# Optimization experiments

Hardware: AMD Instinct MI355X
Metric: run time of the kernel (lower is better)

## Reference

```python
import jax, jax.numpy as jnp
import numpy as np


def setup_inputs() -> dict:
    key = jax.random.key(0)
    k1, k2 = jax.random.split(key)
    B, S, D = 8, 4096, 1024
    E, P = 8, 4
    x = jax.random.normal(k1, (B, S, D), dtype=jnp.float32)
    phi_kernel = jax.random.normal(k2, (D, E * P), dtype=jnp.float32) * (1.0 / np.sqrt(D))
    phi_bias = jnp.zeros((E * P,), dtype=jnp.float32)
    return {"x": x, "phi_kernel": phi_kernel, "phi_bias": phi_bias,
            "num_experts": E, "num_slots": P}


def reference(x, phi_kernel, phi_bias, num_experts, num_slots):
    B, S, D = x.shape
    E, P = num_experts, num_slots
    # phi logits: [B,S,E,P]
    phi_logits = (jnp.einsum('bsd,dk->bsk', x, phi_kernel) + phi_bias).reshape(B, S, E, P)
    # softmax over the sequence axis (each slot is a convex combo of tokens)
    phi_weights = jax.nn.softmax(phi_logits, axis=1)
    # soft slots: weighted sum over tokens -> [B,E,P,D] (fused, no [B,S,E,P,D] blowup)
    soft_slots = jnp.einsum('bsd,bsep->bepd', x, phi_weights)
    expert_inputs = soft_slots.reshape(B, E, P * D)
    expert_weights = jnp.full((B, S, E), 1.0 / E, dtype=x.dtype)
    expert_indices = jnp.broadcast_to(jnp.arange(E, dtype=jnp.int32)[None, None, :], (B, S, E))
    return (expert_weights, expert_indices, phi_weights, soft_slots, expert_inputs)
```

## Files before the change

kernel.cpp:

```cpp
#include <hip/hip_runtime.h>
#include <hip/hip_bf16.h>

#define B 8
#define S 4096
#define DD 1024
#define KK 32

typedef __attribute__((ext_vector_type(8))) short bf16x8;
typedef __attribute__((ext_vector_type(16))) float f32x16;

static __device__ __forceinline__ unsigned short f2bf(float f) {
    unsigned int u = __builtin_bit_cast(unsigned int, f);
    u += 0x7FFFu + ((u >> 16) & 1u);
    return (unsigned short)(u >> 16);
}

static __device__ __forceinline__ unsigned int pack2bf(float lo, float hi) {
    return (unsigned int)f2bf(lo) | ((unsigned int)f2bf(hi) << 16);
}

static __device__ __forceinline__ void gload_lds16(const void* g, void* l) {
    __builtin_amdgcn_global_load_lds(
        (const __attribute__((address_space(1))) unsigned int*)g,
        (__attribute__((address_space(3))) unsigned int*)l, 16, 0, 0);
}

__global__ __launch_bounds__(256) void k0_phit(const float* __restrict__ phi,
                                               unsigned short* __restrict__ phiT) {
    __shared__ float lt[32][33];
    const int d0 = blockIdx.x * 32;
    const int tid = threadIdx.x;
#pragma unroll
    for (int i = 0; i < 4; ++i) {
        int slot = tid + i * 256;
        int d = slot >> 5, k = slot & 31;
        lt[d][k] = phi[(size_t)(d0 + d) * KK + k];
    }
    __syncthreads();
    const int k = tid >> 3, c = tid & 7, d = c * 4;
    short4 pk;
    pk.x = (short)f2bf(lt[d + 0][k]);
    pk.y = (short)f2bf(lt[d + 1][k]);
    pk.z = (short)f2bf(lt[d + 2][k]);
    pk.w = (short)f2bf(lt[d + 3][k]);
    *(short4*)(phiT + (size_t)k * DD + d0 + d) = pk;
}

__global__ __launch_bounds__(256) void k1_logits(const float* __restrict__ x,
                                                 const unsigned short* __restrict__ phiT,
                                                 const float* __restrict__ bias,
                                                 float* __restrict__ lp,
                                                 float* __restrict__ pmax,
                                                 float* __restrict__ psum) {
    __shared__ __align__(16) char sm[65536];

    const int bid = blockIdx.x;
    const int st = bid & 31;
    const int b  = bid >> 5;
    const int tid = threadIdx.x;
    const int wv = __builtin_amdgcn_readfirstlane(tid >> 6);
    const int lane = tid & 63;
    const int l31 = lane & 31;
    const int half = lane >> 5;

    {
        const uint4* pg = (const uint4*)phiT;
#pragma unroll
        for (int i = 0; i < 16; ++i) {
            int slot = tid + i * 256;
            int k = slot >> 7, blk = slot & 127;
            uint4 v = pg[(size_t)k * 128 + blk];
            *(uint4*)(sm + (size_t)k * 2048 + ((blk ^ (k & 7)) << 4)) = v;
        }
    }

    f32x16 acc;
    {
        float bv = bias[l31];
#pragma unroll
        for (int r = 0; r < 16; ++r) acc[r] = bv;
    }
    __syncthreads();

    const float* xg = x + ((size_t)(b * S + st * 128 + wv * 32 + l31)) * DD + half * 8;
    const int kx = l31 & 7;
    const char* brow = sm + (size_t)l31 * 2048;

#pragma unroll 8
    for (int ch = 0; ch < 64; ++ch) {
        float4 a0 = *(const float4*)(xg + ch * 16);
        float4 a1 = *(const float4*)(xg + ch * 16 + 4);
        unsigned int p0 = pack2bf(a0.x, a0.y);
        unsigned int p1 = pack2bf(a0.z, a0.w);
        unsigned int p2 = pack2bf(a1.x, a1.y);
        unsigned int p3 = pack2bf(a1.z, a1.w);
        uint4 pv = make_uint4(p0, p1, p2, p3);
        bf16x8 af = __builtin_bit_cast(bf16x8, pv);
        bf16x8 bfv = *(const bf16x8*)(brow + (((ch * 2 + half) ^ kx) << 4));
        acc = __builtin_amdgcn_mfma_f32_32x32x16_bf16(af, bfv, acc, 0, 0, 0);
    }

    __syncthreads();
    float* lt = (float*)sm;
#pragma unroll
    for (int r = 0; r < 16; ++r) {
        int row = (r & 3) + 8 * (r >> 2) + 4 * half;
        lt[(size_t)l31 * 129 + wv * 32 + row] = acc[r];
    }
    __syncthreads();

    float* o = lp + ((size_t)b * KK) * S + st * 128;
#pragma unroll
    for (int i = 0; i < 4; ++i) {
        int slot = tid + i * 256;
        int k = slot >> 5, s4 = slot & 31;
        float4 v;
        v.x = lt[k * 129 + s4 * 4 + 0];
        v.y = lt[k * 129 + s4 * 4 + 1];
        v.z = lt[k * 129 + s4 * 4 + 2];
        v.w = lt[k * 129 + s4 * 4 + 3];
        *(float4*)(o + (size_t)k * S + s4 * 4) = v;
    }

    const int pk = tid >> 3, pj = tid & 7;
    const float* lr = lt + (size_t)pk * 129 + pj * 16;
    float m = lr[0];
#pragma unroll
    for (int i = 1; i < 16; ++i) m = fmaxf(m, lr[i]);
#pragma unroll
    for (int off = 4; off >= 1; off >>= 1) m = fmaxf(m, __shfl_xor(m, off, 64));
    float l = 0.f;
#pragma unroll
    for (int i = 0; i < 16; ++i) l += __expf(lr[i] - m);
#pragma unroll
    for (int off = 4; off >= 1; off >>= 1) l += __shfl_xor(l, off, 64);
    if (pj == 0) {
        pmax[((size_t)b * KK + pk) * 32 + st] = m;
        psum[((size_t)b * KK + pk) * 32 + st] = l;
    }
}

__global__ __launch_bounds__(256) void k2c_norm(const float* __restrict__ lp,
                                                const float* __restrict__ pmax,
                                                const float* __restrict__ psum,
                                                unsigned short* __restrict__ wbT,
                                                float* __restrict__ pw_out) {
    __shared__ float tile[128][33];
    __shared__ float sM[32], sLinv[32];
    const int b  = blockIdx.x >> 5;
    const int sc = blockIdx.x & 31;
    const int s0 = sc * 128;
    const int tid = threadIdx.x;

    if (tid < 32) {
        const int k = tid;
        float M = -1e30f, L = 0.f;
#pragma unroll
        for (int c = 0; c < 32; ++c) {
            float mc = pmax[((size_t)b * KK + k) * 32 + c];
            float lc = psum[((size_t)b * KK + k) * 32 + c];
            float nM = fmaxf(M, mc);
            L = L * __expf(M - nM) + lc * __expf(mc - nM);
            M = nM;
        }
        sM[k] = M;
        sLinv[k] = 1.0f / L;
    }
    __syncthreads();

    const int sL = tid & 127;
    const int kh = tid >> 7;
#pragma unroll
    for (int kk = 0; kk < 16; ++kk) {
        const int k = kk * 2 + kh;
        const size_t idx = ((size_t)b * KK + k) * S + s0 + sL;
        float v = lp[idx];
        float w = __expf(v - sM[k]) * sLinv[k];
        wbT[idx] = f2bf(w);
        tile[sL][k] = w;
    }
    __syncthreads();

    float* ob = pw_out + ((size_t)b * S + s0) * KK;
#pragma unroll
    for (int i = 0; i < 4; ++i) {
        const int idx4 = tid + i * 256;
        const int sl = idx4 >> 3, kq = idx4 & 7;
        float4 v4 = make_float4(tile[sl][kq * 4 + 0], tile[sl][kq * 4 + 1],
                                tile[sl][kq * 4 + 2], tile[sl][kq * 4 + 3]);
        ((float4*)ob)[idx4] = v4;
    }
}

__global__ __launch_bounds__(256) void k3_slots(const float* __restrict__ x,
                                                const unsigned short* __restrict__ wbT,
                                                float* __restrict__ part) {
    __shared__ __align__(16) char sm[2 * 32768 + 2 * 4096];

    const int bid = blockIdx.x;
    const int sc = bid & 7;
    const int dg = (bid >> 3) & 7;
    const int b  = bid >> 6;
    const int tid = threadIdx.x;
    const int wv = __builtin_amdgcn_readfirstlane(tid >> 6);
    const int lane = tid & 63;
    const int l31 = lane & 31;
    const int half = lane >> 5;

    const char* xsrc = (const char*)(x + ((size_t)(b * S + sc * 512 + wv * 16 + half)) * DD
                                       + dg * 128 + l31 * 4);
    const int wk = wv * 8 + (lane >> 3);
    const char* wsrc = (const char*)wbT + ((size_t)(b * KK + wk) * S + sc * 512) * 2
                                        + (((lane & 7) ^ (wk & 7)) << 4);

    char* const xb0 = sm;
    char* const wb0 = sm + 65536;

    auto stage = [&](int ch, int buf) {
        char* xb = xb0 + buf * 32768 + wv * (16 * 512);
        const char* xs = xsrc + (size_t)ch * (64 * DD * 4);
#pragma unroll
        for (int t = 0; t < 8; ++t)
            gload_lds16(xs + (size_t)t * (2 * DD * 4), xb + t * 1024);
        gload_lds16(wsrc + (size_t)ch * 128, wb0 + buf * 4096 + wv * 1024);
    };

    f32x16 acc;
#pragma unroll
    for (int r = 0; r < 16; ++r) acc[r] = 0.f;

    stage(0, 0);
    __syncthreads();

    const int col = wv * 32 + l31;
    const int kx = l31 & 7;

    for (int ch = 0; ch < 8; ++ch) {
        const int cur = ch & 1;
        if (ch < 7) stage(ch + 1, cur ^ 1);
        const float* xr = (const float*)(xb0 + cur * 32768);
        const char* wr = wb0 + cur * 4096 + (size_t)l31 * 128;
#pragma unroll
        for (int step = 0; step < 4; ++step) {
            bf16x8 af = *(const bf16x8*)(wr + (((step * 2 + half) ^ kx) << 4));
            const int sb = step * 16 + half * 8;
            unsigned int p0 = pack2bf(xr[(sb + 0) * 128 + col], xr[(sb + 1) * 128 + col]);
            unsigned int p1 = pack2bf(xr[(sb + 2) * 128 + col], xr[(sb + 3) * 128 + col]);
            unsigned int p2 = pack2bf(xr[(sb + 4) * 128 + col], xr[(sb + 5) * 128 + col]);
            unsigned int p3 = pack2bf(xr[(sb + 6) * 128 + col], xr[(sb + 7) * 128 + col]);
            uint4 pv = make_uint4(p0, p1, p2, p3);
            bf16x8 bfv = __builtin_bit_cast(bf16x8, pv);
            acc = __builtin_amdgcn_mfma_f32_32x32x16_bf16(af, bfv, acc, 0, 0, 0);
        }
        __syncthreads();
    }

    float* pp = part + (((size_t)sc * B + b) * KK) * DD + dg * 128 + col;
#pragma unroll
    for (int r = 0; r < 16; ++r) {
        int k = (r & 3) + 8 * (r >> 2) + 4 * half;
        pp[(size_t)k * DD] = acc[r];
    }
}

__global__ __launch_bounds__(256) void k4_finalize(const float* __restrict__ part,
                                                   float* __restrict__ out) {
    const int idx = blockIdx.x * 256 + threadIdx.x;
    const float4* p4 = (const float4*)part;

    float4 sv = p4[idx];
#pragma unroll
    for (int c = 1; c < 8; ++c) {
        float4 t = p4[(size_t)c * 65536 + idx];
        sv.x += t.x; sv.y += t.y; sv.z += t.z; sv.w += t.w;
    }

    ((float4*)(out + 1572864))[idx] = sv;
    ((float4*)(out + 1835008))[idx] = sv;
    ((float4*)out)[idx] = make_float4(0.125f, 0.125f, 0.125f, 0.125f);
    float base = (float)((idx * 4) & 7);
    ((float4*)(out + 262144))[idx] = make_float4(base, base + 1.f, base + 2.f, base + 3.f);
}

extern "C" void kernel_launch(void* const* d_in, const int* in_sizes, int n_in,
                              void* d_out, int out_size, void* d_ws, size_t ws_size,
                              hipStream_t stream) {
    const float* x    = (const float*)d_in[0];
    const float* phi  = (const float*)d_in[1];
    const float* bias = (const float*)d_in[2];
    float* out = (float*)d_out;

    float* ws = (float*)d_ws;
    float* lp   = ws;
    float* pmax = ws + 1048576;
    float* psum = ws + 1056768;
    unsigned short* wbT  = (unsigned short*)(ws + 1064960);
    unsigned short* phiT = (unsigned short*)(ws + 1589248);
    float* part = ws + 1605632;
    float* pw_out = out + 524288;

    k0_phit<<<dim3(32), dim3(256), 0, stream>>>(phi, phiT);
    k1_logits<<<dim3(256), dim3(256), 0, stream>>>(x, phiT, bias, lp, pmax, psum);
    k2c_norm<<<dim3(256), dim3(256), 0, stream>>>(lp, pmax, psum, wbT, pw_out);
    k3_slots<<<dim3(512), dim3(256), 0, stream>>>(x, wbT, part);
    k4_finalize<<<dim3(256), dim3(256), 0, stream>>>(part, out);
}
```

Baseline: 235.5 us.

## Split logits kernel over 64-row tiles with split-K across wave pairs

The logits kernel now processes 64 tokens per block instead of 128 and runs twice as many blocks. Within a block, pairs of waves split the D reduction in half and combine their partial results through shared memory. Per-chunk softmax statistics double to 64 chunks, so the normalize kernel now merges them in parallel with 8 lanes per slot and shuffle reductions, and the workspace offsets move to fit. The goal is more blocks to fill the GPU's compute units and shorter per-wave serial loops. The cost is an extra LDS accumulate pass with a barrier, and each block still reloads the full phi tile, now on twice as many blocks.

```diff
diff --git a/kernel.cpp b/kernel.cpp
--- a/kernel.cpp
+++ b/kernel.cpp
@@ -55,13 +55,15 @@
     __shared__ __align__(16) char sm[65536];
 
     const int bid = blockIdx.x;
-    const int st = bid & 31;
-    const int b  = bid >> 5;
+    const int st = bid & 63;
+    const int b  = bid >> 6;
     const int tid = threadIdx.x;
     const int wv = __builtin_amdgcn_readfirstlane(tid >> 6);
     const int lane = tid & 63;
     const int l31 = lane & 31;
     const int half = lane >> 5;
+    const int r0 = (wv >> 1) * 32;
+    const int h  = wv & 1;
 
     {
         const uint4* pg = (const uint4*)phiT;
@@ -76,18 +78,19 @@
 
     f32x16 acc;
     {
-        float bv = bias[l31];
+        float bv = (h == 0) ? bias[l31] : 0.f;
 #pragma unroll
         for (int r = 0; r < 16; ++r) acc[r] = bv;
     }
     __syncthreads();
 
-    const float* xg = x + ((size_t)(b * S + st * 128 + wv * 32 + l31)) * DD + half * 8;
+    const float* xg = x + ((size_t)(b * S + st * 64 + r0 + l31)) * DD
+                        + h * 512 + half * 8;
     const int kx = l31 & 7;
     const char* brow = sm + (size_t)l31 * 2048;
 
 #pragma unroll 8
-    for (int ch = 0; ch < 64; ++ch) {
+    for (int ch = 0; ch < 32; ++ch) {
         float4 a0 = *(const float4*)(xg + ch * 16);
         float4 a1 = *(const float4*)(xg + ch * 16 + 4);
         unsigned int p0 = pack2bf(a0.x, a0.y);
@@ -96,47 +99,58 @@
         unsigned int p3 = pack2bf(a1.z, a1.w);
         uint4 pv = make_uint4(p0, p1, p2, p3);
         bf16x8 af = __builtin_bit_cast(bf16x8, pv);
-        bf16x8 bfv = *(const bf16x8*)(brow + (((ch * 2 + half) ^ kx) << 4));
+        int blk = h * 64 + ch * 2 + half;
+        bf16x8 bfv = *(const bf16x8*)(brow + ((blk ^ kx) << 4));
         acc = __builtin_amdgcn_mfma_f32_32x32x16_bf16(af, bfv, acc, 0, 0, 0);
     }
 
     __syncthreads();
     float* lt = (float*)sm;
-#pragma unroll
-    for (int r = 0; r < 16; ++r) {
-        int row = (r & 3) + 8 * (r >> 2) + 4 * half;
-        lt[(size_t)l31 * 129 + wv * 32 + row] = acc[r];
-    }
-    __syncthreads();
-
-    float* o = lp + ((size_t)b * KK) * S + st * 128;
-#pragma unroll
-    for (int i = 0; i < 4; ++i) {
+    if (h == 0) {
+#pragma unroll
+        for (int r = 0; r < 16; ++r) {
+            int row = (r & 3) + 8 * (r >> 2) + 4 * half;
+            lt[(size_t)l31 * 65 + r0 + row] = acc[r];
+        }
+    }
+    __syncthreads();
+    if (h == 1) {
+#pragma unroll
+        for (int r = 0; r < 16; ++r) {
+            int row = (r & 3) + 8 * (r >> 2) + 4 * half;
+            lt[(size_t)l31 * 65 + r0 + row] += acc[r];
+        }
+    }
+    __syncthreads();
+
+    float* o = lp + ((size_t)b * KK) * S + st * 64;
+#pragma unroll
+    for (int i = 0; i < 2; ++i) {
         int slot = tid + i * 256;
-        int k = slot >> 5, s4 = slot & 31;
+        int k = slot >> 4, s4 = slot & 15;
         float4 v;
-        v.x = lt[k * 129 + s4 * 4 + 0];
-        v.y = lt[k * 129 + s4 * 4 + 1];
-        v.z = lt[k * 129 + s4 * 4 + 2];
-        v.w = lt[k * 129 + s4 * 4 + 3];
+        v.x = lt[k * 65 + s4 * 4 + 0];
+        v.y = lt[k * 65 + s4 * 4 + 1];
+        v.z = lt[k * 65 + s4 * 4 + 2];
+        v.w = lt[k * 65 + s4 * 4 + 3];
         *(float4*)(o + (size_t)k * S + s4 * 4) = v;
     }
 
     const int pk = tid >> 3, pj = tid & 7;
-    const float* lr = lt + (size_t)pk * 129 + pj * 16;
+    const float* lr = lt + (size_t)pk * 65 + pj * 8;
     float m = lr[0];
 #pragma unroll
-    for (int i = 1; i < 16; ++i) m = fmaxf(m, lr[i]);
+    for (int i = 1; i < 8; ++i) m = fmaxf(m, lr[i]);
 #pragma unroll
     for (int off = 4; off >= 1; off >>= 1) m = fmaxf(m, __shfl_xor(m, off, 64));
     float l = 0.f;
 #pragma unroll
-    for (int i = 0; i < 16; ++i) l += __expf(lr[i] - m);
+    for (int i = 0; i < 8; ++i) l += __expf(lr[i] - m);
 #pragma unroll
     for (int off = 4; off >= 1; off >>= 1) l += __shfl_xor(l, off, 64);
     if (pj == 0) {
-        pmax[((size_t)b * KK + pk) * 32 + st] = m;
-        psum[((size_t)b * KK + pk) * 32 + st] = l;
+        pmax[((size_t)b * KK + pk) * 64 + st] = m;
+        psum[((size_t)b * KK + pk) * 64 + st] = l;
     }
 }
 
@@ -152,19 +166,30 @@
     const int s0 = sc * 128;
     const int tid = threadIdx.x;
 
-    if (tid < 32) {
-        const int k = tid;
+    {
+        const int k = tid >> 3, pj = tid & 7;
         float M = -1e30f, L = 0.f;
 #pragma unroll
-        for (int c = 0; c < 32; ++c) {
-            float mc = pmax[((size_t)b * KK + k) * 32 + c];
-            float lc = psum[((size_t)b * KK + k) * 32 + c];
+        for (int c = 0; c < 8; ++c) {
+            int cc = pj * 8 + c;
+            float mc = pmax[((size_t)b * KK + k) * 64 + cc];
+            float lc = psum[((size_t)b * KK + k) * 64 + cc];
             float nM = fmaxf(M, mc);
             L = L * __expf(M - nM) + lc * __expf(mc - nM);
             M = nM;
         }
-        sM[k] = M;
-        sLinv[k] = 1.0f / L;
+#pragma unroll
+        for (int off = 4; off >= 1; off >>= 1) {
+            float Mo = __shfl_xor(M, off, 64);
+            float Lo = __shfl_xor(L, off, 64);
+            float nM = fmaxf(M, Mo);
+            L = L * __expf(M - nM) + Lo * __expf(Mo - nM);
+            M = nM;
+        }
+        if (pj == 0) {
+            sM[k] = M;
+            sLinv[k] = 1.0f / L;
+        }
     }
     __syncthreads();
 
@@ -293,14 +318,14 @@
     float* ws = (float*)d_ws;
     float* lp   = ws;
     float* pmax = ws + 1048576;
-    float* psum = ws + 1056768;
-    unsigned short* wbT  = (unsigned short*)(ws + 1064960);
-    unsigned short* phiT = (unsigned short*)(ws + 1589248);
-    float* part = ws + 1605632;
+    float* psum = ws + 1064960;
+    unsigned short* wbT  = (unsigned short*)(ws + 1081344);
+    unsigned short* phiT = (unsigned short*)(ws + 1605632);
+    float* part = ws + 1622016;
     float* pw_out = out + 524288;
 
     k0_phit<<<dim3(32), dim3(256), 0, stream>>>(phi, phiT);
-    k1_logits<<<dim3(256), dim3(256), 0, stream>>>(x, phiT, bias, lp, pmax, psum);
+    k1_logits<<<dim3(512), dim3(256), 0, stream>>>(x, phiT, bias, lp, pmax, psum);
     k2c_norm<<<dim3(256), dim3(256), 0, stream>>>(lp, pmax, psum, wbT, pw_out);
     k3_slots<<<dim3(512), dim3(256), 0, stream>>>(x, wbT, part);
     k4_finalize<<<dim3(256), dim3(256), 0, stream>>>(part, out);
```

Result: faster. 228.1 us (-3.2%).
